# Optimization experiments

Hardware: AMD Instinct MI355X
Metric: run time of the kernel (lower is better)

Reference implementation:

```python
import jax, jax.numpy as jnp
import numpy as np

B, S, HID = 2, 2048, 2048
NH, NKV, HD = 16, 4, 128  # num_heads, num_kv_heads, head_dim; kqv_size = NH*HD = 2048
KV_DIM = NKV * HD  # 512


def setup_inputs() -> dict:
    key = jax.random.key(0)
    ks = jax.random.split(key, 7)
    sc = 0.02
    return {
        "hidden_states": jax.random.normal(ks[0], (B, S, HID), dtype=jnp.float32),
        "Wq": jax.random.normal(ks[1], (NH * HD, HID), dtype=jnp.float32) * sc,
        "Wk": jax.random.normal(ks[2], (KV_DIM, HID), dtype=jnp.float32) * sc,
        "Wv": jax.random.normal(ks[3], (KV_DIM, HID), dtype=jnp.float32) * sc,
        "Wo": jax.random.normal(ks[4], (HID, NH * HD), dtype=jnp.float32) * sc,
        "bo": jnp.zeros((HID,), dtype=jnp.float32),
    }


def reference(hidden_states, Wq, Wk, Wv, Wo, bo):
    b, s, _ = hidden_states.shape
    # projections (nn.Linear: x @ W.T), no bias on q/k/v
    q = (hidden_states @ Wq.T).reshape(b, s, NH, HD).transpose(0, 2, 1, 3)   # [B,NH,S,HD]
    k = (hidden_states @ Wk.T).reshape(b, s, NKV, HD).transpose(0, 2, 1, 3)  # [B,NKV,S,HD]
    v = (hidden_states @ Wv.T).reshape(b, s, NKV, HD).transpose(0, 2, 1, 3)
    # GQA: query head h uses kv head h // (NH // NKV)
    g = NH // NKV
    k_rep = jnp.repeat(k, g, axis=1)  # [B,NH,S,HD]
    v_rep = jnp.repeat(v, g, axis=1)
    # float32 upcast, NO 1/sqrt(d) scaling (GPT-Neo style)
    qf = q.astype(jnp.float32)
    kf = k_rep.astype(jnp.float32)
    scores = jnp.einsum("bhqd,bhkd->bhqk", qf, kf)  # [B,NH,S,S]
    causal = jnp.tril(jnp.ones((s, s), dtype=bool))[None, None]
    neg = jnp.finfo(scores.dtype).min
    scores = jnp.where(causal, scores, neg)
    attn = jax.nn.softmax(scores, axis=-1).astype(v.dtype)  # dropout p=0 (eval)
    out = jnp.einsum("bhqk,bhkd->bhqd", attn, v_rep)         # [B,NH,S,HD]
    out = out.transpose(0, 2, 1, 3).reshape(b, s, NH * HD)
    return out @ Wo.T + bo
```

## Files before the change

kernel.cpp:

```cpp
#include <hip/hip_runtime.h>

typedef _Float16 f16;
typedef __attribute__((ext_vector_type(4))) _Float16 f16x4;
typedef __attribute__((ext_vector_type(8))) _Float16 f16x8;
typedef __attribute__((ext_vector_type(4))) float f32x4;

#define NB 2
#define NS 2048
#define NHID 2048
#define N_H 16
#define N_KV 4
#define N_HD 128

__device__ __forceinline__ void gload16(void* lds, const void* g) {
  __builtin_amdgcn_global_load_lds(
      (const __attribute__((address_space(1))) unsigned int*)g,
      (__attribute__((address_space(3))) unsigned int*)lds, 16, 0, 0);
}

__global__ __launch_bounds__(256) void cvt_all(
    const float* __restrict__ hs, const float* __restrict__ Wq,
    const float* __restrict__ Wk, const float* __restrict__ Wv,
    const float* __restrict__ Wo, f16* __restrict__ Xh,
    f16* __restrict__ Wqkv, f16* __restrict__ Woh) {
  int i = blockIdx.x * 256 + threadIdx.x;
  const float* src;
  f16* dst;
  int j;
  if (i < 2097152)      { src = hs; dst = Xh;             j = i; }
  else if (i < 3145728) { src = Wq; dst = Wqkv;           j = i - 2097152; }
  else if (i < 3407872) { src = Wk; dst = Wqkv + 4194304; j = i - 3145728; }
  else if (i < 3670016) { src = Wv; dst = Wqkv + 5242880; j = i - 3407872; }
  else                  { src = Wo; dst = Woh;            j = i - 3670016; }
  const float4 v = reinterpret_cast<const float4*>(src)[j];
  f16x4 o = {(f16)v.x, (f16)v.y, (f16)v.z, (f16)v.w};
  reinterpret_cast<f16x4*>(dst)[j] = o;
}

__global__ __launch_bounds__(512, 2) void gemm_qkv(
    const f16* __restrict__ A, const f16* __restrict__ Bm,
    f16* __restrict__ q_out, f16* __restrict__ k_out, f16* __restrict__ v_out) {
  constexpr int K = 2048;
  constexpr int NT = 32;
  __shared__ f16 lds[2][32768];
  const int t = threadIdx.x;
  const int l = t & 63, w = t >> 6;
  const int g = l >> 4, l15 = l & 15;
  const int wr = w >> 2, wc = w & 3;
  const int orig = blockIdx.x;
  const int x = orig & 7, loc = orig >> 3;
  const int mb = (x & 3) * 4 + (loc & 3);
  const int nb = (x >> 2) * 6 + (loc >> 2);
  const f16* Ab = A + (size_t)(mb * 256) * K;
  const f16* Bb = Bm + (size_t)(nb * 256) * K;

  const int rr = ((t >> 5) << 3) | (t & 7);
  const int cc = (t >> 3) & 3;

  auto stageA = [&](int tile, int h) {
    f16* dstbase = lds[tile & 1] + h * 8192;
    size_t so = (size_t)rr * K + tile * 64 + h * 32 + cc * 8;
#pragma unroll
    for (int gi = 0; gi < 2; ++gi)
      gload16(dstbase + gi * 4096 + w * 512, Ab + so + (size_t)(gi * 128) * K);
  };
  auto stageB = [&](int tile, int h) {
    f16* dstbase = lds[tile & 1] + 16384 + h * 8192;
    size_t so = (size_t)rr * K + tile * 64 + h * 32 + cc * 8;
#pragma unroll
    for (int gi = 0; gi < 2; ++gi)
      gload16(dstbase + gi * 4096 + w * 512, Bb + so + (size_t)(gi * 128) * K);
  };
  auto stage_n = [&](int n) {
    if (n >= 4 * NT) return;
    int tile = n >> 2, j = n & 3;
    if (j < 2) stageB(tile, j);
    else       stageA(tile, j - 2);
  };

  const int fragoff = ((l15 >> 3) << 8) + (g << 6) + ((l15 & 7) << 3);
  auto readA = [&](int tile, int mr, int ks) -> f16x8 {
    return *reinterpret_cast<const f16x8*>(
        lds[tile & 1] + ks * 8192 + (wr * 128 + mr * 16) * 32 + fragoff);
  };
  auto readB = [&](int tile, int ni, int ks) -> f16x8 {
    return *reinterpret_cast<const f16x8*>(
        lds[tile & 1] + 16384 + ks * 8192 + (wc * 64 + ni * 16) * 32 + fragoff);
  };

  f32x4 acc[8][4] = {};

#pragma unroll
  for (int n = 0; n < 6; ++n) stage_n(n);
  asm volatile("s_waitcnt vmcnt(4)" ::: "memory");
  __builtin_amdgcn_s_barrier();

  f16x8 bf[4][2];
  for (int T = 0; T < NT; ++T) {
#pragma unroll
    for (int q = 0; q < 4; ++q) {
      if (q == 0 && T > 0) {
        if (T == NT - 1) asm volatile("s_waitcnt vmcnt(0)" ::: "memory");
        else             asm volatile("s_waitcnt vmcnt(4)" ::: "memory");
      }
      f16x8 af[2][2];
#pragma unroll
      for (int i = 0; i < 2; ++i)
#pragma unroll
        for (int ks = 0; ks < 2; ++ks)
          af[i][ks] = readA(T, 2 * q + i, ks);
      if (q == 0) {
#pragma unroll
        for (int ni = 0; ni < 4; ++ni)
#pragma unroll
          for (int ks = 0; ks < 2; ++ks)
            bf[ni][ks] = readB(T, ni, ks);
      }
      stage_n(T * 4 + q + 6);
      if (q == 0) asm volatile("s_waitcnt lgkmcnt(8)" ::: "memory");
      __builtin_amdgcn_s_barrier();
      asm volatile("s_waitcnt lgkmcnt(0)" ::: "memory");
      __builtin_amdgcn_sched_barrier(0);
      __builtin_amdgcn_s_setprio(1);
#pragma unroll
      for (int i = 0; i < 2; ++i)
#pragma unroll
        for (int ni = 0; ni < 4; ++ni)
#pragma unroll
          for (int ks = 0; ks < 2; ++ks)
            acc[2 * q + i][ni] = __builtin_amdgcn_mfma_f32_16x16x32_f16(
                af[i][ks], bf[ni][ks], acc[2 * q + i][ni], 0, 0, 0);
      __builtin_amdgcn_s_setprio(0);
      __builtin_amdgcn_s_barrier();
    }
  }

#pragma unroll
  for (int mi = 0; mi < 8; ++mi) {
    int m0 = mb * 256 + wr * 128 + mi * 16 + 4 * g;
#pragma unroll
    for (int ni = 0; ni < 4; ++ni) {
      int n = nb * 256 + wc * 64 + ni * 16 + l15;
#pragma unroll
      for (int r = 0; r < 4; ++r) {
        int mm = m0 + r;
        float val = acc[mi][ni][r];
        int b = mm >> 11, s = mm & (NS - 1);
        if (n < 2048) {
          int h = n >> 7, d = n & 127;
          q_out[(((size_t)(b * N_H + h)) * NS + s) * N_HD + d] = (f16)val;
        } else if (n < 2560) {
          int n2 = n - 2048, kvh = n2 >> 7, d = n2 & 127;
          k_out[(((size_t)(b * N_KV + kvh)) * NS + s) * N_HD + d] = (f16)val;
        } else {
          int n3 = n - 2560, kvh = n3 >> 7, d = n3 & 127;
          v_out[(((size_t)(b * N_KV + kvh)) * NS + s) * N_HD + d] = (f16)val;
        }
      }
    }
  }
}

template <int MREP>
__global__ __launch_bounds__(512, 2) void gemm8(
    const f16* __restrict__ A, const f16* __restrict__ Bm, const int K,
    float* __restrict__ f_out, const float* __restrict__ bias) {
  constexpr int BM = MREP * 32;
  constexpr int GA = BM / 128;
  constexpr int G = GA + 2;
  constexpr int ATILE = BM * 32;
  constexpr int BTILE = 256 * 32;
  constexpr int BUF = ATILE + BTILE;
  __shared__ f16 lds[4 * BUF];

  const int t = threadIdx.x;
  const int l = t & 63, w = t >> 6;
  const int g = l >> 4, l15 = l & 15;
  const int wr = w >> 2, wc = w & 3;
  const int orig = blockIdx.x;
  const int x = orig & 7, loc = orig >> 3;
  const int mb = (x & 3) * 8 + (loc & 7);
  const int nb = (x >> 2) * 4 + (loc >> 3);
  const int NT = K >> 5;

  const f16* Aorig = A + (size_t)(mb * BM) * K;
  const f16* Borig = Bm + (size_t)(nb * 256) * K;

  size_t offA[GA], offB[2];
#pragma unroll
  for (int gi = 0; gi < GA; ++gi) {
    int beta = gi * 8192 + t * 16;
    int r = ((beta >> 9) << 3) | ((beta >> 4) & 7);
    int c = (beta >> 7) & 3;
    offA[gi] = (size_t)r * K + c * 8;
  }
#pragma unroll
  for (int gj = 0; gj < 2; ++gj) {
    int beta = gj * 8192 + t * 16;
    int r = ((beta >> 9) << 3) | ((beta >> 4) & 7);
    int c = (beta >> 7) & 3;
    offB[gj] = (size_t)r * K + c * 8;
  }

  auto stage = [&](int kt, int gi) {
    f16* bufbase = lds + (kt & 3) * BUF;
    if (gi < GA) {
      gload16(bufbase + gi * 4096 + w * 512, Aorig + offA[gi] + kt * 32);
    } else {
      int gj = gi - GA;
      gload16(bufbase + ATILE + gj * 4096 + w * 512, Borig + offB[gj] + kt * 32);
    }
  };
  const int fragoff = ((l15 >> 3) << 8) + (g << 6) + ((l15 & 7) << 3);
  auto readA = [&](int kt, int mi) -> f16x8 {
    int R0 = wr * (MREP * 16) + mi * 16;
    return *reinterpret_cast<const f16x8*>(lds + (kt & 3) * BUF + R0 * 32 + fragoff);
  };
  auto readB = [&](int kt, int ni) -> f16x8 {
    int R0 = wc * 64 + ni * 16;
    return *reinterpret_cast<const f16x8*>(lds + (kt & 3) * BUF + ATILE + R0 * 32 + fragoff);
  };

  f32x4 acc[MREP][4] = {};

#pragma unroll
  for (int pt = 0; pt < 3; ++pt)
#pragma unroll
    for (int gi = 0; gi < G; ++gi) stage(pt, gi);
  asm volatile("s_waitcnt vmcnt(6)" ::: "memory");
  __builtin_amdgcn_s_barrier();

  for (int kt = 0; kt < NT; ++kt) {
    f16x8 af[4], bf[4];
#pragma unroll
    for (int mi = 0; mi < 4; ++mi) af[mi] = readA(kt, mi);
#pragma unroll
    for (int ni = 0; ni < 4; ++ni) bf[ni] = readB(kt, ni);
    if (kt + 3 < NT) {
      stage(kt + 3, 0);
      stage(kt + 3, 1);
      stage(kt + 3, 2);
      asm volatile("s_waitcnt vmcnt(6)" ::: "memory");
    } else if (kt + 2 < NT) {
      asm volatile("s_waitcnt vmcnt(3)" ::: "memory");
    } else if (kt + 1 < NT) {
      asm volatile("s_waitcnt vmcnt(0)" ::: "memory");
    }
    __builtin_amdgcn_s_barrier();
    asm volatile("s_waitcnt lgkmcnt(0)" ::: "memory");
    __builtin_amdgcn_s_setprio(1);
#pragma unroll
    for (int mi = 0; mi < 4; ++mi)
#pragma unroll
      for (int ni = 0; ni < 4; ++ni)
        acc[mi][ni] = __builtin_amdgcn_mfma_f32_16x16x32_f16(af[mi], bf[ni], acc[mi][ni], 0, 0, 0);
    __builtin_amdgcn_s_setprio(0);
    __builtin_amdgcn_s_barrier();
  }

#pragma unroll
  for (int mi = 0; mi < MREP; ++mi) {
    int m0 = mb * BM + wr * (MREP * 16) + mi * 16 + 4 * g;
#pragma unroll
    for (int ni = 0; ni < 4; ++ni) {
      int n = nb * 256 + wc * 64 + ni * 16 + l15;
#pragma unroll
      for (int r = 0; r < 4; ++r)
        f_out[(size_t)(m0 + r) * NHID + n] = acc[mi][ni][r] + bias[n];
    }
  }
}

__global__ __launch_bounds__(256) void transpose_v(const f16* __restrict__ V,
                                                   f16* __restrict__ Vt) {
  __shared__ f16 tt[64][72];
  int s0 = blockIdx.x * 64, d0 = blockIdx.y * 64, bk = blockIdx.z;
  const f16* Vp = V + (size_t)bk * NS * N_HD;
  f16* Vtp = Vt + (size_t)bk * N_HD * NS;
  int tid = threadIdx.x;
#pragma unroll
  for (int it = 0; it < 2; ++it) {
    int c = it * 256 + tid;
    int sr = c >> 3, dc = (c & 7) * 8;
    f16x8 v = *reinterpret_cast<const f16x8*>(Vp + (size_t)(s0 + sr) * N_HD + d0 + dc);
#pragma unroll
    for (int j = 0; j < 8; ++j) tt[dc + j][sr] = v[j];
  }
  __syncthreads();
#pragma unroll
  for (int it = 0; it < 2; ++it) {
    int c = it * 256 + tid;
    int dr = c >> 3, sc = (c & 7) * 8;
    f16x8 o;
#pragma unroll
    for (int j = 0; j < 8; ++j) o[j] = tt[dr][sc + j];
    *reinterpret_cast<f16x8*>(Vtp + (size_t)(d0 + dr) * NS + s0 + sc) = o;
  }
}

__device__ __forceinline__ void stage_kv(const f16* __restrict__ Kp,
                                         const f16* __restrict__ Vp,
                                         f16* Kl, f16* Vl, int kt, int w, int l) {
#pragma unroll
  for (int it = 0; it < 4; ++it) {
    int cb = (it * 4 + w) * 64;
    int c = cb + l;
    int krow = c >> 4, pch = c & 15;
    int sch = (pch & 8) | ((pch ^ krow) & 7);
    gload16(Kl + cb * 8, Kp + (size_t)(kt * 64 + krow) * N_HD + sch * 8);
  }
#pragma unroll
  for (int it = 0; it < 4; ++it) {
    int cb = (it * 4 + w) * 64;
    int c = cb + l;
    int drow = c >> 3, pch = c & 7;
    int sch = (pch ^ drow) & 7;
    gload16(Vl + cb * 8, Vp + (size_t)drow * NS + kt * 64 + sch * 8);
  }
}

__device__ __forceinline__ void attn_step(
    const f16x8* qf, f32x4* oacc, float* mrow, float* lrow, int q0, int kt,
    const f16* Kl, const f16* Vl, f16* Pw, int g, int l15, bool diag) {
  f32x4 sacc[4];
#pragma unroll
  for (int nt = 0; nt < 4; ++nt) {
    f32x4 z = {0.f, 0.f, 0.f, 0.f};
#pragma unroll
    for (int ks = 0; ks < 4; ++ks) {
      int kr = nt * 16 + l15;
      int ch = ks * 4 + g;
      int sw = (ch & 8) | ((ch ^ kr) & 7);
      f16x8 kf = *reinterpret_cast<const f16x8*>(Kl + kr * 128 + sw * 8);
      z = __builtin_amdgcn_mfma_f32_16x16x32_f16(qf[ks], kf, z, 0, 0, 0);
    }
    sacc[nt] = z;
  }

  float p[4][4];
#pragma unroll
  for (int r = 0; r < 4; ++r) {
    int qg = q0 + r;
    float m = -3.0e38f;
#pragma unroll
    for (int nt = 0; nt < 4; ++nt) {
      float sv = sacc[nt][r];
      if (diag) {
        int kg = kt * 64 + nt * 16 + l15;
        if (kg > qg) sv = -3.0e38f;
      }
      p[nt][r] = sv;
      m = fmaxf(m, sv);
    }
#pragma unroll
    for (int off = 8; off >= 1; off >>= 1) m = fmaxf(m, __shfl_xor(m, off));
    float m2 = fmaxf(mrow[r], m);
    float alpha = __builtin_amdgcn_exp2f(mrow[r] - m2);
    mrow[r] = m2;
    lrow[r] *= alpha;
#pragma unroll
    for (int nt = 0; nt < 4; ++nt)
      p[nt][r] = __builtin_amdgcn_exp2f(p[nt][r] - m2);
#pragma unroll
    for (int dt = 0; dt < 8; ++dt) oacc[dt][r] *= alpha;
  }

#pragma unroll
  for (int nt = 0; nt < 4; ++nt)
#pragma unroll
    for (int r = 0; r < 4; ++r) {
      int ql = 4 * g + r;
      int kp = nt * 16 + l15;
      int ch = kp >> 3;
      int idx = ql * 64 + (ch ^ (ql & 7)) * 8 + (kp & 7);
      Pw[idx] = (f16)p[nt][r];
    }
  asm volatile("s_waitcnt lgkmcnt(0)" ::: "memory");
  __builtin_amdgcn_sched_barrier(0);

  f16x8 pa[2];
#pragma unroll
  for (int ks2 = 0; ks2 < 2; ++ks2) {
    int ch = ks2 * 4 + g;
    pa[ks2] = *reinterpret_cast<const f16x8*>(&Pw[l15 * 64 + (ch ^ (l15 & 7)) * 8]);
  }
  const f16x8 ones = {(f16)1.f, (f16)1.f, (f16)1.f, (f16)1.f,
                      (f16)1.f, (f16)1.f, (f16)1.f, (f16)1.f};
  f32x4 lacc = {0.f, 0.f, 0.f, 0.f};
#pragma unroll
  for (int ks2 = 0; ks2 < 2; ++ks2)
    lacc = __builtin_amdgcn_mfma_f32_16x16x32_f16(pa[ks2], ones, lacc, 0, 0, 0);
#pragma unroll
  for (int dt = 0; dt < 8; ++dt)
#pragma unroll
    for (int ks2 = 0; ks2 < 2; ++ks2) {
      int d = dt * 16 + l15;
      int ch = ks2 * 4 + g;
      f16x8 vf = *reinterpret_cast<const f16x8*>(Vl + d * 64 + (ch ^ (d & 7)) * 8);
      oacc[dt] = __builtin_amdgcn_mfma_f32_16x16x32_f16(pa[ks2], vf, oacc[dt], 0, 0, 0);
    }
#pragma unroll
  for (int r = 0; r < 4; ++r) lrow[r] += lacc[r];
}

__global__ __launch_bounds__(256, 2) void attn_kernel(
    const f16* __restrict__ Q, const f16* __restrict__ K,
    const f16* __restrict__ Vt, f16* __restrict__ O) {
  __shared__ f16 Klds[2][64 * 128];
  __shared__ f16 Vlds[2][128 * 64];
  __shared__ f16 Plds[4][16 * 64];
  const int t = threadIdx.x, l = t & 63, w = t >> 6;
  const int g = l >> 4, l15 = l & 15;
  const int orig = blockIdx.x;
  const int x = orig & 7, loc = orig >> 3;
  const int b = x >> 2, kvh = x & 3;
  const int h = kvh * 4 + (loc & 3);
  const int pi = loc >> 2;
  const int qtA = pi, qtB = 31 - pi;
  const f16* Qp = Q + ((size_t)(b * N_H + h)) * NS * N_HD;
  const f16* Kp = K + ((size_t)(b * N_KV + kvh)) * NS * N_HD;
  const f16* Vp = Vt + ((size_t)(b * N_KV + kvh)) * N_HD * NS;

  const f16 l2e = (f16)1.44269504f;
  f16x8 qfA[4], qfB[4];
  const int qrA = qtA * 64 + w * 16 + l15;
  const int qrB = qtB * 64 + w * 16 + l15;
#pragma unroll
  for (int ks = 0; ks < 4; ++ks) {
    qfA[ks] = *reinterpret_cast<const f16x8*>(Qp + (size_t)qrA * N_HD + ks * 32 + g * 8);
    qfB[ks] = *reinterpret_cast<const f16x8*>(Qp + (size_t)qrB * N_HD + ks * 32 + g * 8);
#pragma unroll
    for (int j = 0; j < 8; ++j) { qfA[ks][j] *= l2e; qfB[ks][j] *= l2e; }
  }

  f32x4 oA[8] = {}, oB[8] = {};
  float mA[4], lAr[4], mB[4], lBr[4];
#pragma unroll
  for (int r = 0; r < 4; ++r) {
    mA[r] = -3.0e38f; lAr[r] = 0.f;
    mB[r] = -3.0e38f; lBr[r] = 0.f;
  }
  const int q0A = qtA * 64 + w * 16 + 4 * g;
  const int q0B = qtB * 64 + w * 16 + 4 * g;

  const int nkt = qtB + 1;
  stage_kv(Kp, Vp, Klds[0], Vlds[0], 0, w, l);
  asm volatile("s_waitcnt vmcnt(0)" ::: "memory");
  __syncthreads();
  int cur = 0;
  for (int kt = 0; kt < nkt; ++kt) {
    if (kt + 1 < nkt)
      stage_kv(Kp, Vp, Klds[cur ^ 1], Vlds[cur ^ 1], kt + 1, w, l);
    attn_step(qfB, oB, mB, lBr, q0B, kt, Klds[cur], Vlds[cur], Plds[w], g, l15, kt == qtB);
    if (kt <= qtA)
      attn_step(qfA, oA, mA, lAr, q0A, kt, Klds[cur], Vlds[cur], Plds[w], g, l15, kt == qtA);
    asm volatile("s_waitcnt vmcnt(0)" ::: "memory");
    __syncthreads();
    cur ^= 1;
  }

#pragma unroll
  for (int r = 0; r < 4; ++r) {
    float invB = 1.0f / lBr[r];
    f16* orowB = O + (size_t)(b * NS + q0B + r) * NHID + h * N_HD;
#pragma unroll
    for (int dt = 0; dt < 8; ++dt) orowB[dt * 16 + l15] = (f16)(oB[dt][r] * invB);
    float invA = 1.0f / lAr[r];
    f16* orowA = O + (size_t)(b * NS + q0A + r) * NHID + h * N_HD;
#pragma unroll
    for (int dt = 0; dt < 8; ++dt) orowA[dt * 16 + l15] = (f16)(oA[dt][r] * invA);
  }
}

extern "C" void kernel_launch(void* const* d_in, const int* in_sizes, int n_in,
                              void* d_out, int out_size, void* d_ws, size_t ws_size,
                              hipStream_t stream) {
  const float* hs = (const float*)d_in[0];
  const float* Wq = (const float*)d_in[1];
  const float* Wk = (const float*)d_in[2];
  const float* Wv = (const float*)d_in[3];
  const float* Wo = (const float*)d_in[4];
  const float* bo = (const float*)d_in[5];
  float* out = (float*)d_out;

  char* ws = (char*)d_ws;
  f16* Xh   = (f16*)(ws);
  f16* Wqkv = (f16*)(ws + 16777216);
  f16* Woh  = (f16*)(ws + 29360128);
  f16* Qb   = (f16*)(ws + 37748736);
  f16* Kb   = (f16*)(ws + 54525952);
  f16* Vb   = (f16*)(ws + 58720256);
  f16* Vtb  = (f16*)(ws + 62914560);
  f16* Ob   = Xh;

  cvt_all<<<18432, 256, 0, stream>>>(hs, Wq, Wk, Wv, Wo, Xh, Wqkv, Woh);
  gemm_qkv<<<192, 512, 0, stream>>>(Xh, Wqkv, Qb, Kb, Vb);
  transpose_v<<<dim3(32, 2, 8), 256, 0, stream>>>(Vb, Vtb);
  attn_kernel<<<512, 256, 0, stream>>>(Qb, Kb, Vtb, Ob);
  gemm8<4><<<256, 512, 0, stream>>>(Ob, Woh, 2048, out, bo);
}
```

Measured before the change: 212.8 us.

## Fuse V transpose into QKV GEMM epilogue and retile both GEMMs

The QKV projection GEMM now writes V directly in transposed layout from its epilogue, removing the separate transpose_v kernel and the intermediate V buffer. Its tile changes from 256x256 to 256x192, giving 256 blocks so the grid fills all compute units, with a reworked 64-wide K double-buffer pipeline. The output projection GEMM is rewritten with a 128x256 tile and a 2-stage, 64-wide K pipeline in place of the 4-stage 32-wide one. The costs are uncoalesced 8-byte stores into transposed V and a shallower prefetch depth in the output GEMM.

```diff
diff --git a/kernel.cpp b/kernel.cpp
--- a/kernel.cpp
+++ b/kernel.cpp
@@ -39,10 +39,10 @@
 
 __global__ __launch_bounds__(512, 2) void gemm_qkv(
     const f16* __restrict__ A, const f16* __restrict__ Bm,
-    f16* __restrict__ q_out, f16* __restrict__ k_out, f16* __restrict__ v_out) {
+    f16* __restrict__ q_out, f16* __restrict__ k_out, f16* __restrict__ vt_out) {
   constexpr int K = 2048;
   constexpr int NT = 32;
-  __shared__ f16 lds[2][32768];
+  __shared__ f16 lds[2][28672];
   const int t = threadIdx.x;
   const int l = t & 63, w = t >> 6;
   const int g = l >> 4, l15 = l & 15;
@@ -50,74 +50,70 @@
   const int orig = blockIdx.x;
   const int x = orig & 7, loc = orig >> 3;
   const int mb = (x & 3) * 4 + (loc & 3);
-  const int nb = (x >> 2) * 6 + (loc >> 2);
+  const int nb = (x >> 2) * 8 + (loc >> 2);
   const f16* Ab = A + (size_t)(mb * 256) * K;
-  const f16* Bb = Bm + (size_t)(nb * 256) * K;
+  const f16* Bb = Bm + (size_t)(nb * 192) * K;
 
   const int rr = ((t >> 5) << 3) | (t & 7);
   const int cc = (t >> 3) & 3;
-
-  auto stageA = [&](int tile, int h) {
-    f16* dstbase = lds[tile & 1] + h * 8192;
-    size_t so = (size_t)rr * K + tile * 64 + h * 32 + cc * 8;
-#pragma unroll
-    for (int gi = 0; gi < 2; ++gi)
-      gload16(dstbase + gi * 4096 + w * 512, Ab + so + (size_t)(gi * 128) * K);
+  const int dstw = w * 512;
+  int srcB[3];
+#pragma unroll
+  for (int j = 0; j < 3; ++j) {
+    int db0 = j * 4096 + t * 8;
+    int h = (db0 >= 6144) ? 1 : 0;
+    int u = (db0 - h * 6144) >> 3;
+    int rowB = ((u >> 5) << 3) | (u & 7);
+    int ccB = (u >> 3) & 3;
+    srcB[j] = rowB * K + h * 32 + ccB * 8;
+  }
+
+  auto stageA = [&](int tile, int j) {
+    int h = j >> 1, gi = j & 1;
+    gload16(&lds[tile & 1][h * 8192 + gi * 4096 + dstw],
+            Ab + (size_t)(gi * 128 + rr) * K + tile * 64 + h * 32 + cc * 8);
   };
-  auto stageB = [&](int tile, int h) {
-    f16* dstbase = lds[tile & 1] + 16384 + h * 8192;
-    size_t so = (size_t)rr * K + tile * 64 + h * 32 + cc * 8;
-#pragma unroll
-    for (int gi = 0; gi < 2; ++gi)
-      gload16(dstbase + gi * 4096 + w * 512, Bb + so + (size_t)(gi * 128) * K);
+  auto stageB = [&](int tile, int j) {
+    gload16(&lds[tile & 1][16384 + j * 4096 + dstw],
+            Bb + (size_t)srcB[j] + tile * 64);
   };
-  auto stage_n = [&](int n) {
-    if (n >= 4 * NT) return;
-    int tile = n >> 2, j = n & 3;
-    if (j < 2) stageB(tile, j);
-    else       stageA(tile, j - 2);
-  };
 
   const int fragoff = ((l15 >> 3) << 8) + (g << 6) + ((l15 & 7) << 3);
-  auto readA = [&](int tile, int mr, int ks) -> f16x8 {
-    return *reinterpret_cast<const f16x8*>(
-        lds[tile & 1] + ks * 8192 + (wr * 128 + mr * 16) * 32 + fragoff);
-  };
-  auto readB = [&](int tile, int ni, int ks) -> f16x8 {
-    return *reinterpret_cast<const f16x8*>(
-        lds[tile & 1] + 16384 + ks * 8192 + (wc * 64 + ni * 16) * 32 + fragoff);
-  };
-
-  f32x4 acc[8][4] = {};
-
-#pragma unroll
-  for (int n = 0; n < 6; ++n) stage_n(n);
-  asm volatile("s_waitcnt vmcnt(4)" ::: "memory");
+  f32x4 acc[8][3] = {};
+
+#pragma unroll
+  for (int j = 0; j < 3; ++j) stageB(0, j);
+#pragma unroll
+  for (int j = 0; j < 4; ++j) stageA(0, j);
+#pragma unroll
+  for (int j = 0; j < 3; ++j) stageB(1, j);
+  asm volatile("s_waitcnt vmcnt(3)" ::: "memory");
   __builtin_amdgcn_s_barrier();
 
-  f16x8 bf[4][2];
+  f16x8 bf[3][2];
   for (int T = 0; T < NT; ++T) {
+    const f16* buf = lds[T & 1];
 #pragma unroll
     for (int q = 0; q < 4; ++q) {
-      if (q == 0 && T > 0) {
-        if (T == NT - 1) asm volatile("s_waitcnt vmcnt(0)" ::: "memory");
-        else             asm volatile("s_waitcnt vmcnt(4)" ::: "memory");
-      }
       f16x8 af[2][2];
 #pragma unroll
       for (int i = 0; i < 2; ++i)
 #pragma unroll
         for (int ks = 0; ks < 2; ++ks)
-          af[i][ks] = readA(T, 2 * q + i, ks);
+          af[i][ks] = *reinterpret_cast<const f16x8*>(
+              buf + ks * 8192 + (wr * 128 + (2 * q + i) * 16) * 32 + fragoff);
       if (q == 0) {
 #pragma unroll
-        for (int ni = 0; ni < 4; ++ni)
+        for (int ni = 0; ni < 3; ++ni)
 #pragma unroll
           for (int ks = 0; ks < 2; ++ks)
-            bf[ni][ks] = readB(T, ni, ks);
-      }
-      stage_n(T * 4 + q + 6);
-      if (q == 0) asm volatile("s_waitcnt lgkmcnt(8)" ::: "memory");
+            bf[ni][ks] = *reinterpret_cast<const f16x8*>(
+                buf + 16384 + ks * 6144 + (wc * 48 + ni * 16) * 32 + fragoff);
+      }
+      if (q == 0)      { if (T + 1 < NT) { stageA(T + 1, 0); stageA(T + 1, 1); } }
+      else if (q == 1) { if (T + 1 < NT) { stageA(T + 1, 2); stageA(T + 1, 3); } }
+      else if (q == 2) { if (T + 2 < NT) { stageB(T + 2, 0); stageB(T + 2, 1); } }
+      else             { if (T + 2 < NT) { stageB(T + 2, 2); } }
       __builtin_amdgcn_s_barrier();
       asm volatile("s_waitcnt lgkmcnt(0)" ::: "memory");
       __builtin_amdgcn_sched_barrier(0);
@@ -125,12 +121,16 @@
 #pragma unroll
       for (int i = 0; i < 2; ++i)
 #pragma unroll
-        for (int ni = 0; ni < 4; ++ni)
+        for (int ni = 0; ni < 3; ++ni)
 #pragma unroll
           for (int ks = 0; ks < 2; ++ks)
             acc[2 * q + i][ni] = __builtin_amdgcn_mfma_f32_16x16x32_f16(
                 af[i][ks], bf[ni][ks], acc[2 * q + i][ni], 0, 0, 0);
       __builtin_amdgcn_s_setprio(0);
+      if (q == 3 && T + 1 < NT) {
+        if (T + 2 < NT) asm volatile("s_waitcnt vmcnt(3)" ::: "memory");
+        else            asm volatile("s_waitcnt vmcnt(0)" ::: "memory");
+      }
       __builtin_amdgcn_s_barrier();
     }
   }
@@ -138,41 +138,37 @@
 #pragma unroll
   for (int mi = 0; mi < 8; ++mi) {
     int m0 = mb * 256 + wr * 128 + mi * 16 + 4 * g;
-#pragma unroll
-    for (int ni = 0; ni < 4; ++ni) {
-      int n = nb * 256 + wc * 64 + ni * 16 + l15;
-#pragma unroll
-      for (int r = 0; r < 4; ++r) {
-        int mm = m0 + r;
-        float val = acc[mi][ni][r];
-        int b = mm >> 11, s = mm & (NS - 1);
-        if (n < 2048) {
-          int h = n >> 7, d = n & 127;
-          q_out[(((size_t)(b * N_H + h)) * NS + s) * N_HD + d] = (f16)val;
-        } else if (n < 2560) {
-          int n2 = n - 2048, kvh = n2 >> 7, d = n2 & 127;
-          k_out[(((size_t)(b * N_KV + kvh)) * NS + s) * N_HD + d] = (f16)val;
-        } else {
-          int n3 = n - 2560, kvh = n3 >> 7, d = n3 & 127;
-          v_out[(((size_t)(b * N_KV + kvh)) * NS + s) * N_HD + d] = (f16)val;
-        }
-      }
-    }
-  }
-}
-
-template <int MREP>
-__global__ __launch_bounds__(512, 2) void gemm8(
-    const f16* __restrict__ A, const f16* __restrict__ Bm, const int K,
+    int b = m0 >> 11, s0 = m0 & (NS - 1);
+#pragma unroll
+    for (int ni = 0; ni < 3; ++ni) {
+      int n = nb * 192 + wc * 48 + ni * 16 + l15;
+      if (n < 2048) {
+        int h = n >> 7, d = n & 127;
+        f16* qp = q_out + (((size_t)(b * N_H + h)) * NS + s0) * N_HD + d;
+#pragma unroll
+        for (int r = 0; r < 4; ++r) qp[r * N_HD] = (f16)acc[mi][ni][r];
+      } else if (n < 2560) {
+        int n2 = n - 2048, kvh = n2 >> 7, d = n2 & 127;
+        f16* kp = k_out + (((size_t)(b * N_KV + kvh)) * NS + s0) * N_HD + d;
+#pragma unroll
+        for (int r = 0; r < 4; ++r) kp[r * N_HD] = (f16)acc[mi][ni][r];
+      } else {
+        int n3 = n - 2560, kvh = n3 >> 7, d = n3 & 127;
+        f16x4 o4 = {(f16)acc[mi][ni][0], (f16)acc[mi][ni][1],
+                    (f16)acc[mi][ni][2], (f16)acc[mi][ni][3]};
+        *reinterpret_cast<f16x4*>(
+            vt_out + (((size_t)(b * N_KV + kvh)) * N_HD + d) * NS + s0) = o4;
+      }
+    }
+  }
+}
+
+__global__ __launch_bounds__(512, 2) void gemm_out(
+    const f16* __restrict__ A, const f16* __restrict__ Bm,
     float* __restrict__ f_out, const float* __restrict__ bias) {
-  constexpr int BM = MREP * 32;
-  constexpr int GA = BM / 128;
-  constexpr int G = GA + 2;
-  constexpr int ATILE = BM * 32;
-  constexpr int BTILE = 256 * 32;
-  constexpr int BUF = ATILE + BTILE;
-  __shared__ f16 lds[4 * BUF];
-
+  constexpr int K = 2048;
+  constexpr int NT = 32;
+  __shared__ f16 lds[2][24576];
   const int t = threadIdx.x;
   const int l = t & 63, w = t >> 6;
   const int g = l >> 4, l15 = l & 15;
@@ -181,86 +177,83 @@
   const int x = orig & 7, loc = orig >> 3;
   const int mb = (x & 3) * 8 + (loc & 7);
   const int nb = (x >> 2) * 4 + (loc >> 3);
-  const int NT = K >> 5;
-
-  const f16* Aorig = A + (size_t)(mb * BM) * K;
-  const f16* Borig = Bm + (size_t)(nb * 256) * K;
-
-  size_t offA[GA], offB[2];
-#pragma unroll
-  for (int gi = 0; gi < GA; ++gi) {
-    int beta = gi * 8192 + t * 16;
-    int r = ((beta >> 9) << 3) | ((beta >> 4) & 7);
-    int c = (beta >> 7) & 3;
-    offA[gi] = (size_t)r * K + c * 8;
-  }
-#pragma unroll
-  for (int gj = 0; gj < 2; ++gj) {
-    int beta = gj * 8192 + t * 16;
-    int r = ((beta >> 9) << 3) | ((beta >> 4) & 7);
-    int c = (beta >> 7) & 3;
-    offB[gj] = (size_t)r * K + c * 8;
-  }
-
-  auto stage = [&](int kt, int gi) {
-    f16* bufbase = lds + (kt & 3) * BUF;
-    if (gi < GA) {
-      gload16(bufbase + gi * 4096 + w * 512, Aorig + offA[gi] + kt * 32);
-    } else {
-      int gj = gi - GA;
-      gload16(bufbase + ATILE + gj * 4096 + w * 512, Borig + offB[gj] + kt * 32);
-    }
+  const f16* Ab = A + (size_t)(mb * 128) * K;
+  const f16* Bb = Bm + (size_t)(nb * 256) * K;
+
+  const int rr = ((t >> 5) << 3) | (t & 7);
+  const int cc = (t >> 3) & 3;
+  const int dstw = w * 512;
+
+  auto stageA = [&](int tile, int h) {
+    gload16(&lds[tile & 1][h * 4096 + dstw],
+            Ab + (size_t)rr * K + tile * 64 + h * 32 + cc * 8);
   };
+  auto stageB = [&](int tile, int j) {
+    int h = j >> 1, gi = j & 1;
+    gload16(&lds[tile & 1][8192 + h * 8192 + gi * 4096 + dstw],
+            Bb + (size_t)(gi * 128 + rr) * K + tile * 64 + h * 32 + cc * 8);
+  };
+
   const int fragoff = ((l15 >> 3) << 8) + (g << 6) + ((l15 & 7) << 3);
-  auto readA = [&](int kt, int mi) -> f16x8 {
-    int R0 = wr * (MREP * 16) + mi * 16;
-    return *reinterpret_cast<const f16x8*>(lds + (kt & 3) * BUF + R0 * 32 + fragoff);
-  };
-  auto readB = [&](int kt, int ni) -> f16x8 {
-    int R0 = wc * 64 + ni * 16;
-    return *reinterpret_cast<const f16x8*>(lds + (kt & 3) * BUF + ATILE + R0 * 32 + fragoff);
-  };
-
-  f32x4 acc[MREP][4] = {};
-
-#pragma unroll
-  for (int pt = 0; pt < 3; ++pt)
-#pragma unroll
-    for (int gi = 0; gi < G; ++gi) stage(pt, gi);
-  asm volatile("s_waitcnt vmcnt(6)" ::: "memory");
+  f32x4 acc[4][4] = {};
+
+  stageA(0, 0); stageA(0, 1);
+#pragma unroll
+  for (int j = 0; j < 4; ++j) stageB(0, j);
+#pragma unroll
+  for (int j = 0; j < 4; ++j) stageB(1, j);
+  asm volatile("s_waitcnt vmcnt(4)" ::: "memory");
   __builtin_amdgcn_s_barrier();
 
-  for (int kt = 0; kt < NT; ++kt) {
-    f16x8 af[4], bf[4];
-#pragma unroll
-    for (int mi = 0; mi < 4; ++mi) af[mi] = readA(kt, mi);
-#pragma unroll
-    for (int ni = 0; ni < 4; ++ni) bf[ni] = readB(kt, ni);
-    if (kt + 3 < NT) {
-      stage(kt + 3, 0);
-      stage(kt + 3, 1);
-      stage(kt + 3, 2);
-      asm volatile("s_waitcnt vmcnt(6)" ::: "memory");
-    } else if (kt + 2 < NT) {
-      asm volatile("s_waitcnt vmcnt(3)" ::: "memory");
-    } else if (kt + 1 < NT) {
-      asm volatile("s_waitcnt vmcnt(0)" ::: "memory");
-    }
-    __builtin_amdgcn_s_barrier();
-    asm volatile("s_waitcnt lgkmcnt(0)" ::: "memory");
-    __builtin_amdgcn_s_setprio(1);
-#pragma unroll
-    for (int mi = 0; mi < 4; ++mi)
-#pragma unroll
-      for (int ni = 0; ni < 4; ++ni)
-        acc[mi][ni] = __builtin_amdgcn_mfma_f32_16x16x32_f16(af[mi], bf[ni], acc[mi][ni], 0, 0, 0);
-    __builtin_amdgcn_s_setprio(0);
-    __builtin_amdgcn_s_barrier();
-  }
-
-#pragma unroll
-  for (int mi = 0; mi < MREP; ++mi) {
-    int m0 = mb * BM + wr * (MREP * 16) + mi * 16 + 4 * g;
+  f16x8 bf[4][2];
+  for (int T = 0; T < NT; ++T) {
+    const f16* buf = lds[T & 1];
+#pragma unroll
+    for (int q = 0; q < 2; ++q) {
+      f16x8 af[2][2];
+#pragma unroll
+      for (int i = 0; i < 2; ++i)
+#pragma unroll
+        for (int ks = 0; ks < 2; ++ks)
+          af[i][ks] = *reinterpret_cast<const f16x8*>(
+              buf + ks * 4096 + (wr * 64 + (2 * q + i) * 16) * 32 + fragoff);
+      if (q == 0) {
+#pragma unroll
+        for (int ni = 0; ni < 4; ++ni)
+#pragma unroll
+          for (int ks = 0; ks < 2; ++ks)
+            bf[ni][ks] = *reinterpret_cast<const f16x8*>(
+                buf + 8192 + ks * 8192 + (wc * 64 + ni * 16) * 32 + fragoff);
+      }
+      if (q == 0) {
+        if (T + 1 < NT) { stageA(T + 1, 0); stageA(T + 1, 1); }
+      } else {
+        if (T + 2 < NT) { stageB(T + 2, 0); stageB(T + 2, 1); stageB(T + 2, 2); stageB(T + 2, 3); }
+      }
+      __builtin_amdgcn_s_barrier();
+      asm volatile("s_waitcnt lgkmcnt(0)" ::: "memory");
+      __builtin_amdgcn_sched_barrier(0);
+      __builtin_amdgcn_s_setprio(1);
+#pragma unroll
+      for (int i = 0; i < 2; ++i)
+#pragma unroll
+        for (int ni = 0; ni < 4; ++ni)
+#pragma unroll
+          for (int ks = 0; ks < 2; ++ks)
+            acc[2 * q + i][ni] = __builtin_amdgcn_mfma_f32_16x16x32_f16(
+                af[i][ks], bf[ni][ks], acc[2 * q + i][ni], 0, 0, 0);
+      __builtin_amdgcn_s_setprio(0);
+      if (q == 1 && T + 1 < NT) {
+        if (T + 2 < NT) asm volatile("s_waitcnt vmcnt(4)" ::: "memory");
+        else            asm volatile("s_waitcnt vmcnt(0)" ::: "memory");
+      }
+      __builtin_amdgcn_s_barrier();
+    }
+  }
+
+#pragma unroll
+  for (int mi = 0; mi < 4; ++mi) {
+    int m0 = mb * 128 + wr * 64 + mi * 16 + 4 * g;
 #pragma unroll
     for (int ni = 0; ni < 4; ++ni) {
       int n = nb * 256 + wc * 64 + ni * 16 + l15;
@@ -268,33 +261,6 @@
       for (int r = 0; r < 4; ++r)
         f_out[(size_t)(m0 + r) * NHID + n] = acc[mi][ni][r] + bias[n];
     }
-  }
-}
-
-__global__ __launch_bounds__(256) void transpose_v(const f16* __restrict__ V,
-                                                   f16* __restrict__ Vt) {
-  __shared__ f16 tt[64][72];
-  int s0 = blockIdx.x * 64, d0 = blockIdx.y * 64, bk = blockIdx.z;
-  const f16* Vp = V + (size_t)bk * NS * N_HD;
-  f16* Vtp = Vt + (size_t)bk * N_HD * NS;
-  int tid = threadIdx.x;
-#pragma unroll
-  for (int it = 0; it < 2; ++it) {
-    int c = it * 256 + tid;
-    int sr = c >> 3, dc = (c & 7) * 8;
-    f16x8 v = *reinterpret_cast<const f16x8*>(Vp + (size_t)(s0 + sr) * N_HD + d0 + dc);
-#pragma unroll
-    for (int j = 0; j < 8; ++j) tt[dc + j][sr] = v[j];
-  }
-  __syncthreads();
-#pragma unroll
-  for (int it = 0; it < 2; ++it) {
-    int c = it * 256 + tid;
-    int dr = c >> 3, sc = (c & 7) * 8;
-    f16x8 o;
-#pragma unroll
-    for (int j = 0; j < 8; ++j) o[j] = tt[dr][sc + j];
-    *reinterpret_cast<f16x8*>(Vtp + (size_t)(d0 + dr) * NS + s0 + sc) = o;
   }
 }
 
@@ -489,13 +455,11 @@
   f16* Woh  = (f16*)(ws + 29360128);
   f16* Qb   = (f16*)(ws + 37748736);
   f16* Kb   = (f16*)(ws + 54525952);
-  f16* Vb   = (f16*)(ws + 58720256);
   f16* Vtb  = (f16*)(ws + 62914560);
   f16* Ob   = Xh;
 
   cvt_all<<<18432, 256, 0, stream>>>(hs, Wq, Wk, Wv, Wo, Xh, Wqkv, Woh);
-  gemm_qkv<<<192, 512, 0, stream>>>(Xh, Wqkv, Qb, Kb, Vb);
-  transpose_v<<<dim3(32, 2, 8), 256, 0, stream>>>(Vb, Vtb);
+  gemm_qkv<<<256, 512, 0, stream>>>(Xh, Wqkv, Qb, Kb, Vtb);
   attn_kernel<<<512, 256, 0, stream>>>(Qb, Kb, Vtb, Ob);
-  gemm8<4><<<256, 512, 0, stream>>>(Ob, Woh, 2048, out, bo);
-}
+  gemm_out<<<256, 512, 0, stream>>>(Ob, Woh, out, bo);
+}
```

New measurement: 203.8 us, median of 2. 4.3% less time.
